# Kernel optimization log

Hardware: AMD Instinct MI355X
Metric: run time of the kernel (lower is better)

Reference implementation:

```python
import jax, jax.numpy as jnp
import numpy as np

N = 50000          # num nodes
E = 800000         # num edges (avg degree 16)
D_IN = 128         # input_size
H = 128            # hidden_size
BN_EPS = 1e-5


def setup_inputs() -> dict:
    key = jax.random.key(0)
    ks = jax.random.split(key, 16)
    std = 1.0 / np.sqrt(H)
    u = lambda k, shape: jax.random.uniform(k, shape, jnp.float32, -std, std)
    return {
        "x": jax.random.normal(ks[0], (N, D_IN), jnp.float32),
        "hx": jax.random.normal(ks[1], (N, H), jnp.float32),
        "cx": jax.random.normal(ks[2], (N, H), jnp.float32),
        "edge_src": jax.random.randint(ks[3], (E,), 0, N, jnp.int32),
        "edge_dst": jax.random.randint(ks[4], (E,), 0, N, jnp.int32),
        "edge_weight": jax.random.uniform(ks[5], (E,), jnp.float32) / 16.0,  # ~normalized adj values
        "gcn_weight": u(ks[6], (D_IN, H)),
        "bias": u(ks[7], (H,)),
        "x2h_w": u(ks[8], (4 * H, H)),
        "x2h_b": u(ks[9], (4 * H,)),
        "h2h_w": u(ks[10], (4 * H, H)),
        "h2h_b": u(ks[11], (4 * H,)),
        "bn_gamma": u(ks[12], (H,)),
        "bn_beta": u(ks[13], (H,)),
        "bn_mean": jnp.zeros((H,), jnp.float32),
        "bn_var": jnp.ones((H,), jnp.float32),
    }


def reference(x, hx, cx, edge_src, edge_dst, edge_weight, gcn_weight, bias,
              x2h_w, x2h_b, h2h_w, h2h_b, bn_gamma, bn_beta, bn_mean, bn_var):
    # GCN: support = x @ W, then sparse adj @ support via gather/segment-sum
    support = x @ gcn_weight                                   # (N, H)
    msgs = edge_weight[:, None] * support[edge_src]            # (E, H)
    agg = jax.ops.segment_sum(msgs, edge_dst, num_segments=N)  # (N, H) = spmm(adj, support)
    h = jax.nn.relu(agg)
    # dropout: eval mode -> identity
    h = h + bias
    # BatchNorm1d (eval mode, running stats)
    h = (h - bn_mean) * jax.lax.rsqrt(bn_var + BN_EPS) * bn_gamma + bn_beta
    # fused LSTM gates: x2h(h) + h2h(hx)
    gates = h @ x2h_w.T + x2h_b + hx @ h2h_w.T + h2h_b         # (N, 4H)
    i_g, f_g, g_g, o_g = jnp.split(gates, 4, axis=1)
    cy = cx * jax.nn.sigmoid(f_g) + jax.nn.sigmoid(i_g) * jnp.tanh(g_g)
    hy = jax.nn.sigmoid(o_g) * jnp.tanh(cy)
    return hy, cy
```

## Files before the change

### kernel.cpp

```cpp
#include <hip/hip_runtime.h>

#define NN 50000
#define NE 800000
#define HH 128
#define BN_EPS 1e-5f
#define SCAN_NB ((NN + 255) / 256)

typedef unsigned short u16;
typedef unsigned int u32;
typedef short bf16x8 __attribute__((ext_vector_type(8)));
typedef float f32x4 __attribute__((ext_vector_type(4)));

static __device__ __forceinline__ float bf2f(u16 u){
  union { u32 i; float f; } v; v.i = ((u32)u) << 16; return v.f;
}
static __device__ __forceinline__ u16 f2bf(float f){
  union { float f; u32 i; } v; v.f = f;
  u32 x = v.i;
  return (u16)((x + 0x7fffu + ((x >> 16) & 1u)) >> 16);
}
static __device__ __forceinline__ float sigm(float x){
  return 1.f / (1.f + __expf(-x));
}
static __device__ __forceinline__ float tanh_fast(float x){
  return 1.f - 2.f / (1.f + __expf(2.f * x));
}


__global__ void hist_kernel(const int* __restrict__ dst, int* __restrict__ counts, int E){
  int e = blockIdx.x * blockDim.x + threadIdx.x;
  if (e < E) atomicAdd(&counts[dst[e]], 1);
}


__global__ __launch_bounds__(256) void scan_bsum(
    const int* __restrict__ counts, int* __restrict__ bsums, int n){
  int i = blockIdx.x * 256 + threadIdx.x;
  int v = (i < n) ? counts[i] : 0;
#pragma unroll
  for (int off = 1; off < 64; off <<= 1) v += __shfl_xor(v, off);
  __shared__ int ws[4];
  if ((threadIdx.x & 63) == 0) ws[threadIdx.x >> 6] = v;
  __syncthreads();
  if (threadIdx.x == 0) bsums[blockIdx.x] = ws[0] + ws[1] + ws[2] + ws[3];
}

__global__ __launch_bounds__(256) void scan_tops(int* __restrict__ bsums, int nb){
  __shared__ int sh[256];
  int t = threadIdx.x;
  int v = (t < nb) ? bsums[t] : 0;
  sh[t] = v;
  __syncthreads();
  for (int off = 1; off < 256; off <<= 1){
    int u = (t >= off) ? sh[t - off] : 0;
    __syncthreads();
    sh[t] += u;
    __syncthreads();
  }
  if (t < nb) bsums[t] = sh[t] - v;
}

__global__ __launch_bounds__(256) void scan_final(
    const int* __restrict__ counts, const int* __restrict__ bsums,
    int* __restrict__ offs, int* __restrict__ cursor, int n){
  __shared__ int sh[256];
  int t = threadIdx.x;
  int i = blockIdx.x * 256 + t;
  int v = (i < n) ? counts[i] : 0;
  sh[t] = v;
  __syncthreads();
  for (int off = 1; off < 256; off <<= 1){
    int u = (t >= off) ? sh[t - off] : 0;
    __syncthreads();
    sh[t] += u;
    __syncthreads();
  }
  int excl = sh[t] - v + bsums[blockIdx.x];
  if (i < n){ offs[i] = excl; cursor[i] = excl; }
}

__global__ void scatter_kernel(const int* __restrict__ src, const int* __restrict__ dst,
                               const float* __restrict__ w, int* __restrict__ cursor,
                               int2* __restrict__ esw, int E){
  int e = blockIdx.x * blockDim.x + threadIdx.x;
  if (e < E){
    int d = dst[e];
    int pos = atomicAdd(&cursor[d], 1);
    esw[pos] = make_int2(src[e], __float_as_int(w[e]));
  }
}

__global__ void prep_pack(const float* __restrict__ x2hw, const float* __restrict__ h2hw,
                          const float* __restrict__ x2hb, const float* __restrict__ h2hb,
                          const float* __restrict__ gcnw,
                          u16* __restrict__ wcat, u16* __restrict__ wgcn,
                          float* __restrict__ bsum){
  int i = blockIdx.x * blockDim.x + threadIdx.x;
  int n = i >> 8, k = i & 255;
  float v = (k < 128) ? x2hw[n * 128 + k] : h2hw[n * 128 + (k - 128)];
  int nt = n >> 4, lc = n & 15;
  int kk = k >> 5, lq = (k >> 3) & 3, e = k & 7;
  wcat[(((nt * 8 + kk) * 64) + lq * 16 + lc) * 8 + e] = f2bf(v);
  if (i < 16384){
    int nn = i >> 7, kx = i & 127;
    wgcn[i] = f2bf(gcnw[kx * 128 + nn]);
  }
  if (i < 512) bsum[i] = x2hb[i] + h2hb[i];
}

__global__ __launch_bounds__(256) void support_mfma(
    const float* __restrict__ x, const u16* __restrict__ wgcn,
    u16* __restrict__ support, int N){
  int tid = threadIdx.x;
  int wave = tid >> 6, lane = tid & 63;
  int c = lane & 15, q = lane >> 4;
  int row0 = blockIdx.x * 64 + wave * 16;
  int arow = row0 + c; if (arow > N - 1) arow = N - 1;
  f32x4 acc[8];
#pragma unroll
  for (int t = 0; t < 8; t++) acc[t] = (f32x4){0.f, 0.f, 0.f, 0.f};

  const u16* wp = wgcn + (size_t)c * 128 + q * 8;
#pragma unroll
  for (int k0 = 0; k0 < 128; k0 += 32){
    const float* ap = x + (size_t)arow * 128 + k0 + q * 8;
    float4 f0 = *(const float4*)ap;
    float4 f1 = *(const float4*)(ap + 4);
    u16 tmp[8] = {f2bf(f0.x), f2bf(f0.y), f2bf(f0.z), f2bf(f0.w),
                  f2bf(f1.x), f2bf(f1.y), f2bf(f1.z), f2bf(f1.w)};
    bf16x8 afrag = *(bf16x8*)tmp;
#pragma unroll
    for (int t = 0; t < 8; t++){
      bf16x8 bfrag = *(const bf16x8*)(wp + (size_t)t * 16 * 128 + k0);
      acc[t] = __builtin_amdgcn_mfma_f32_16x16x32_bf16(afrag, bfrag, acc[t], 0, 0, 0);
    }
  }
#pragma unroll
  for (int t = 0; t < 8; t++){
#pragma unroll
    for (int j = 0; j < 4; j++){
      int r = row0 + q * 4 + j;
      if (r < N) support[(size_t)r * 128 + t * 16 + c] = f2bf(acc[t][j]);
    }
  }
}

__global__ __launch_bounds__(256) void agg_bn2(
    const u16* __restrict__ support, const int2* __restrict__ esw,
    const int* __restrict__ offs, const int* __restrict__ counts,
    const float* __restrict__ bias, const float* __restrict__ gamma,
    const float* __restrict__ beta, const float* __restrict__ mean,
    const float* __restrict__ var, const float* __restrict__ hx,
    u16* __restrict__ hbn, u16* __restrict__ hxb, int N){
  int wid = blockIdx.x * 4 + (threadIdx.x >> 6);
  int lane = threadIdx.x & 63;
  if (wid >= N) return;
  int c = lane * 2;
  float2 hv = *(const float2*)(hx + (size_t)wid * HH + c);
  int start = offs[wid];
  int deg   = counts[wid];
  float a0 = 0.f, a1 = 0.f;
  for (int base = 0; base < deg; base += 64){
    int cnt = deg - base; if (cnt > 64) cnt = 64;
    int2 my = make_int2(0, 0);
    if (lane < cnt) my = esw[start + base + lane];
    int e = 0;
    for (; e + 8 <= cnt; e += 8){
      int s[8]; float g[8]; u32 u[8];
#pragma unroll
      for (int k = 0; k < 8; k++){
        s[k] = __shfl(my.x, e + k);
        g[k] = __int_as_float(__shfl(my.y, e + k));
      }
#pragma unroll
      for (int k = 0; k < 8; k++)
        u[k] = *(const u32*)(support + (size_t)s[k] * HH + c);
#pragma unroll
      for (int k = 0; k < 8; k++){
        a0 = fmaf(g[k], bf2f((u16)(u[k] & 0xffffu)), a0);
        a1 = fmaf(g[k], bf2f((u16)(u[k] >> 16)), a1);
      }
    }
    for (; e + 4 <= cnt; e += 4){
      int s[4]; float g[4]; u32 u[4];
#pragma unroll
      for (int k = 0; k < 4; k++){
        s[k] = __shfl(my.x, e + k);
        g[k] = __int_as_float(__shfl(my.y, e + k));
      }
#pragma unroll
      for (int k = 0; k < 4; k++)
        u[k] = *(const u32*)(support + (size_t)s[k] * HH + c);
#pragma unroll
      for (int k = 0; k < 4; k++){
        a0 = fmaf(g[k], bf2f((u16)(u[k] & 0xffffu)), a0);
        a1 = fmaf(g[k], bf2f((u16)(u[k] >> 16)), a1);
      }
    }
    for (; e < cnt; e++){
      int   si = __shfl(my.x, e);
      float gi = __int_as_float(__shfl(my.y, e));
      u32 ui = *(const u32*)(support + (size_t)si * HH + c);
      a0 = fmaf(gi, bf2f((u16)(ui & 0xffffu)), a0);
      a1 = fmaf(gi, bf2f((u16)(ui >> 16)), a1);
    }
  }
  float h0 = fmaxf(a0, 0.f) + bias[c];
  float h1 = fmaxf(a1, 0.f) + bias[c + 1];
  float s0 = gamma[c]     * rsqrtf(var[c]     + BN_EPS);
  float s1 = gamma[c + 1] * rsqrtf(var[c + 1] + BN_EPS);
  float r0 = (h0 - mean[c])     * s0 + beta[c];
  float r1 = (h1 - mean[c + 1]) * s1 + beta[c + 1];
  u32 pack = (u32)f2bf(r0) | ((u32)f2bf(r1) << 16);
  *(u32*)(hbn + (size_t)wid * HH + c) = pack;
  u32 hp = (u32)f2bf(hv.x) | ((u32)f2bf(hv.y) << 16);
  *(u32*)(hxb + (size_t)wid * HH + c) = hp;
}

__global__ __launch_bounds__(1024, 1) void gates_mfma6(
    const u16* __restrict__ hbn, const u16* __restrict__ hxb,
    const u16* __restrict__ wcat, const float* __restrict__ bsum,
    const float* __restrict__ cx, float* __restrict__ out, int N){
  __shared__ float lbuf[2][8][16][64];
  int tid = threadIdx.x;
  int wave = tid >> 6, lane = tid & 63;
  int c = lane & 15, q = lane >> 4;
  int cw = wave & 7, kh = wave >> 3;
  int hloc = cw * 16 + c;

  const bf16x8* wsrc = (const bf16x8*)wcat;
  bf16x8 btile[4][4];
#pragma unroll
  for (int g = 0; g < 4; g++)
#pragma unroll
    for (int kk = 0; kk < 4; kk++)
      btile[g][kk] = wsrc[((size_t)((g * 8 + cw) * 8) + kh * 4 + kk) * 64 + lane];

  float bi = 0.f, bf_ = 0.f, bg = 0.f, bo = 0.f;
  if (kh == 0){
    bi  = bsum[hloc];
    bf_ = bsum[128 + hloc];
    bg  = bsum[256 + hloc];
    bo  = bsum[384 + hloc];
  }
  const u16* abuf = kh ? hxb : hbn;
  const size_t NH = (size_t)N * HH;
  const int nchunk = N >> 4;
  int p = 0;
  int chunk = blockIdx.x;

  bf16x8 a_cur[4];
  if (chunk < nchunk){
    const u16* ap = abuf + (size_t)((chunk << 4) + c) * 128 + q * 8;
#pragma unroll
    for (int kk = 0; kk < 4; kk++) a_cur[kk] = *(const bf16x8*)(ap + kk * 32);
  }

  for (; chunk < nchunk; chunk += gridDim.x){
    int row0 = chunk << 4;
    int nxt = chunk + gridDim.x;
    int prow = (nxt < nchunk) ? (nxt << 4) : 0;
    const u16* pnp = abuf + (size_t)(prow + c) * 128 + q * 8;
    bf16x8 a_nxt[4];
#pragma unroll
    for (int kk = 0; kk < 4; kk++) a_nxt[kk] = *(const bf16x8*)(pnp + kk * 32);
    float cxv[4];
    if (kh == 0){
#pragma unroll
      for (int j = 0; j < 4; j++)
        cxv[j] = cx[(size_t)(row0 + q * 4 + j) * HH + hloc];
    }

    f32x4 acc[4];
#pragma unroll
    for (int g = 0; g < 4; g++) acc[g] = (f32x4){0.f, 0.f, 0.f, 0.f};
#pragma unroll
    for (int kk = 0; kk < 4; kk++){
#pragma unroll
      for (int g = 0; g < 4; g++)
        acc[g] = __builtin_amdgcn_mfma_f32_16x16x32_bf16(a_cur[kk], btile[g][kk], acc[g], 0, 0, 0);
    }
    if (kh == 1){
#pragma unroll
      for (int g = 0; g < 4; g++)
#pragma unroll
        for (int j = 0; j < 4; j++)
          lbuf[p][cw][g * 4 + j][lane] = acc[g][j];
    }
    __syncthreads();
    if (kh == 0){
#pragma unroll
      for (int j = 0; j < 4; j++){
        int r = row0 + q * 4 + j;
        float gi = acc[0][j] + lbuf[p][cw][0 + j][lane]  + bi;
        float gf = acc[1][j] + lbuf[p][cw][4 + j][lane]  + bf_;
        float gg = acc[2][j] + lbuf[p][cw][8 + j][lane]  + bg;
        float go = acc[3][j] + lbuf[p][cw][12 + j][lane] + bo;
        float is = sigm(gi), fs = sigm(gf), gt = tanh_fast(gg), os = sigm(go);
        float cyv = cxv[j] * fs + is * gt;
        out[(size_t)r * HH + hloc]      = os * tanh_fast(cyv);
        out[NH + (size_t)r * HH + hloc] = cyv;
      }
    }
#pragma unroll
    for (int kk = 0; kk < 4; kk++) a_cur[kk] = a_nxt[kk];
    p ^= 1;
  }
}


extern "C" void kernel_launch(void* const* d_in, const int* in_sizes, int n_in,
                              void* d_out, int out_size, void* d_ws, size_t ws_size,
                              hipStream_t stream){
  const float* x     = (const float*)d_in[0];
  const float* hx    = (const float*)d_in[1];
  const float* cx    = (const float*)d_in[2];
  const int*   esrc  = (const int*)d_in[3];
  const int*   edst  = (const int*)d_in[4];
  const float* ew    = (const float*)d_in[5];
  const float* gcn_w = (const float*)d_in[6];
  const float* bias  = (const float*)d_in[7];
  const float* x2hw  = (const float*)d_in[8];
  const float* x2hb  = (const float*)d_in[9];
  const float* h2hw  = (const float*)d_in[10];
  const float* h2hb  = (const float*)d_in[11];
  const float* bn_g  = (const float*)d_in[12];
  const float* bn_b  = (const float*)d_in[13];
  const float* bn_m  = (const float*)d_in[14];
  const float* bn_v  = (const float*)d_in[15];
  float* out = (float*)d_out;

  char* w = (char*)d_ws;
  u16* support = (u16*)w; w += (((size_t)NN * HH * 2) + 255) & ~(size_t)255;
  u16* hbn     = (u16*)w; w += (((size_t)NN * HH * 2) + 255) & ~(size_t)255;
  u16* hxb     = (u16*)w; w += (((size_t)NN * HH * 2) + 255) & ~(size_t)255;
  int* counts  = (int*)w; w += (((size_t)NN * 4) + 255) & ~(size_t)255;
  int* offs    = (int*)w; w += (((size_t)NN * 4) + 255) & ~(size_t)255;
  int* cursor  = (int*)w; w += (((size_t)NN * 4) + 255) & ~(size_t)255;
  int* bsums   = (int*)w; w += (((size_t)SCAN_NB * 4) + 255) & ~(size_t)255;
  int2* esw    = (int2*)w; w += (((size_t)NE * 8) + 255) & ~(size_t)255;
  u16* wcat    = (u16*)w; w += (((size_t)512 * 256 * 2) + 255) & ~(size_t)255;
  u16* wgcn    = (u16*)w; w += (((size_t)128 * 128 * 2) + 255) & ~(size_t)255;
  float* bsum  = (float*)w; w += (((size_t)512 * 4) + 255) & ~(size_t)255;

  hipMemsetAsync(counts, 0, (size_t)NN * 4, stream);
  prep_pack<<<512, 256, 0, stream>>>(x2hw, h2hw, x2hb, h2hb, gcn_w, wcat, wgcn, bsum);
  hist_kernel<<<(NE + 255) / 256, 256, 0, stream>>>(edst, counts, NE);
  scan_bsum<<<SCAN_NB, 256, 0, stream>>>(counts, bsums, NN);
  scan_tops<<<1, 256, 0, stream>>>(bsums, SCAN_NB);
  scan_final<<<SCAN_NB, 256, 0, stream>>>(counts, bsums, offs, cursor, NN);
  scatter_kernel<<<(NE + 255) / 256, 256, 0, stream>>>(esrc, edst, ew, cursor, esw, NE);
  support_mfma<<<(NN + 63) / 64, 256, 0, stream>>>(x, wgcn, support, NN);
  agg_bn2<<<(NN + 3) / 4, 256, 0, stream>>>(support, esw, offs, counts,
                                            bias, bn_g, bn_b, bn_m, bn_v, hx, hbn, hxb, NN);
  gates_mfma6<<<256, 1024, 0, stream>>>(hbn, hxb, wcat, bsum, cx, out, NN);
}
```

Measured before the change: 350.2 us.

## Fold counts zeroing into prep kernel, use broadcast edge loads, double gates grid

Drops the separate memset by zeroing the degree counts inside prep_pack, which launches 131072 threads, more than the node count. The aggregation kernel now has every lane load each edge record directly as a uniform broadcast load, replacing the per-64-edge cooperative load plus shuffles. The gates kernel launch grows from 256 to 512 blocks of 1024 threads, which changes occupancy and work split and assumes the kernel handles the larger grid correctly. The direct loads add redundant memory traffic across lanes, though they hit in cache.

```diff
diff --git a/kernel.cpp b/kernel.cpp
--- a/kernel.cpp
+++ b/kernel.cpp
@@ -94,7 +94,7 @@
                           const float* __restrict__ x2hb, const float* __restrict__ h2hb,
                           const float* __restrict__ gcnw,
                           u16* __restrict__ wcat, u16* __restrict__ wgcn,
-                          float* __restrict__ bsum){
+                          float* __restrict__ bsum, int* __restrict__ counts){
   int i = blockIdx.x * blockDim.x + threadIdx.x;
   int n = i >> 8, k = i & 255;
   float v = (k < 128) ? x2hw[n * 128 + k] : h2hw[n * 128 + (k - 128)];
@@ -106,6 +106,7 @@
     wgcn[i] = f2bf(gcnw[kx * 128 + nn]);
   }
   if (i < 512) bsum[i] = x2hb[i] + h2hb[i];
+  if (i < NN) counts[i] = 0;
 }
 
 __global__ __launch_bounds__(256) void support_mfma(
@@ -145,7 +146,7 @@
   }
 }
 
-__global__ __launch_bounds__(256) void agg_bn2(
+__global__ __launch_bounds__(256) void agg_bn3(
     const u16* __restrict__ support, const int2* __restrict__ esw,
     const int* __restrict__ offs, const int* __restrict__ counts,
     const float* __restrict__ bias, const float* __restrict__ gamma,
@@ -160,50 +161,41 @@
   int start = offs[wid];
   int deg   = counts[wid];
   float a0 = 0.f, a1 = 0.f;
-  for (int base = 0; base < deg; base += 64){
-    int cnt = deg - base; if (cnt > 64) cnt = 64;
-    int2 my = make_int2(0, 0);
-    if (lane < cnt) my = esw[start + base + lane];
-    int e = 0;
-    for (; e + 8 <= cnt; e += 8){
-      int s[8]; float g[8]; u32 u[8];
-#pragma unroll
-      for (int k = 0; k < 8; k++){
-        s[k] = __shfl(my.x, e + k);
-        g[k] = __int_as_float(__shfl(my.y, e + k));
-      }
-#pragma unroll
-      for (int k = 0; k < 8; k++)
-        u[k] = *(const u32*)(support + (size_t)s[k] * HH + c);
-#pragma unroll
-      for (int k = 0; k < 8; k++){
-        a0 = fmaf(g[k], bf2f((u16)(u[k] & 0xffffu)), a0);
-        a1 = fmaf(g[k], bf2f((u16)(u[k] >> 16)), a1);
-      }
-    }
-    for (; e + 4 <= cnt; e += 4){
-      int s[4]; float g[4]; u32 u[4];
-#pragma unroll
-      for (int k = 0; k < 4; k++){
-        s[k] = __shfl(my.x, e + k);
-        g[k] = __int_as_float(__shfl(my.y, e + k));
-      }
-#pragma unroll
-      for (int k = 0; k < 4; k++)
-        u[k] = *(const u32*)(support + (size_t)s[k] * HH + c);
-#pragma unroll
-      for (int k = 0; k < 4; k++){
-        a0 = fmaf(g[k], bf2f((u16)(u[k] & 0xffffu)), a0);
-        a1 = fmaf(g[k], bf2f((u16)(u[k] >> 16)), a1);
-      }
-    }
-    for (; e < cnt; e++){
-      int   si = __shfl(my.x, e);
-      float gi = __int_as_float(__shfl(my.y, e));
-      u32 ui = *(const u32*)(support + (size_t)si * HH + c);
-      a0 = fmaf(gi, bf2f((u16)(ui & 0xffffu)), a0);
-      a1 = fmaf(gi, bf2f((u16)(ui >> 16)), a1);
-    }
+  int e = 0;
+  for (; e + 8 <= deg; e += 8){
+    int2 ev[8]; u32 u[8];
+#pragma unroll
+    for (int k = 0; k < 8; k++) ev[k] = esw[start + e + k];
+#pragma unroll
+    for (int k = 0; k < 8; k++)
+      u[k] = *(const u32*)(support + (size_t)ev[k].x * HH + c);
+#pragma unroll
+    for (int k = 0; k < 8; k++){
+      float g = __int_as_float(ev[k].y);
+      a0 = fmaf(g, bf2f((u16)(u[k] & 0xffffu)), a0);
+      a1 = fmaf(g, bf2f((u16)(u[k] >> 16)), a1);
+    }
+  }
+  for (; e + 4 <= deg; e += 4){
+    int2 ev[4]; u32 u[4];
+#pragma unroll
+    for (int k = 0; k < 4; k++) ev[k] = esw[start + e + k];
+#pragma unroll
+    for (int k = 0; k < 4; k++)
+      u[k] = *(const u32*)(support + (size_t)ev[k].x * HH + c);
+#pragma unroll
+    for (int k = 0; k < 4; k++){
+      float g = __int_as_float(ev[k].y);
+      a0 = fmaf(g, bf2f((u16)(u[k] & 0xffffu)), a0);
+      a1 = fmaf(g, bf2f((u16)(u[k] >> 16)), a1);
+    }
+  }
+  for (; e < deg; e++){
+    int2 ev = esw[start + e];
+    float g = __int_as_float(ev.y);
+    u32 ui = *(const u32*)(support + (size_t)ev.x * HH + c);
+    a0 = fmaf(g, bf2f((u16)(ui & 0xffffu)), a0);
+    a1 = fmaf(g, bf2f((u16)(ui >> 16)), a1);
   }
   float h0 = fmaxf(a0, 0.f) + bias[c];
   float h1 = fmaxf(a1, 0.f) + bias[c + 1];
@@ -343,15 +335,14 @@
   u16* wgcn    = (u16*)w; w += (((size_t)128 * 128 * 2) + 255) & ~(size_t)255;
   float* bsum  = (float*)w; w += (((size_t)512 * 4) + 255) & ~(size_t)255;
 
-  hipMemsetAsync(counts, 0, (size_t)NN * 4, stream);
-  prep_pack<<<512, 256, 0, stream>>>(x2hw, h2hw, x2hb, h2hb, gcn_w, wcat, wgcn, bsum);
+  prep_pack<<<512, 256, 0, stream>>>(x2hw, h2hw, x2hb, h2hb, gcn_w, wcat, wgcn, bsum, counts);
   hist_kernel<<<(NE + 255) / 256, 256, 0, stream>>>(edst, counts, NE);
   scan_bsum<<<SCAN_NB, 256, 0, stream>>>(counts, bsums, NN);
   scan_tops<<<1, 256, 0, stream>>>(bsums, SCAN_NB);
   scan_final<<<SCAN_NB, 256, 0, stream>>>(counts, bsums, offs, cursor, NN);
   scatter_kernel<<<(NE + 255) / 256, 256, 0, stream>>>(esrc, edst, ew, cursor, esw, NE);
   support_mfma<<<(NN + 63) / 64, 256, 0, stream>>>(x, wgcn, support, NN);
-  agg_bn2<<<(NN + 3) / 4, 256, 0, stream>>>(support, esw, offs, counts,
+  agg_bn3<<<(NN + 3) / 4, 256, 0, stream>>>(support, esw, offs, counts,
                                             bias, bn_g, bn_b, bn_m, bn_v, hx, hbn, hxb, NN);
-  gates_mfma6<<<256, 1024, 0, stream>>>(hbn, hxb, wcat, bsum, cx, out, NN);
-}
+  gates_mfma6<<<512, 1024, 0, stream>>>(hbn, hxb, wcat, bsum, cx, out, NN);
+}
```

Result: slower. 360.6 us (+3.0%).
